# Kernel optimization log

Measured on AMD Instinct MI355X. Metric: run time of the kernel, lower is better.

Reference implementation:

```python
import jax, jax.numpy as jnp
import numpy as np

N = 100000
F = 128
H = 16
C = 40
E = 3200000


def _gcn_norm(edge_index, num_nodes):
    # add self-loops, compute symmetric normalization (PyG GCNConv default)
    loops = jnp.arange(num_nodes, dtype=edge_index.dtype)
    src = jnp.concatenate([edge_index[0], loops])
    dst = jnp.concatenate([edge_index[1], loops])
    ones = jnp.ones(src.shape[0], dtype=jnp.float32)
    deg = jax.ops.segment_sum(ones, dst, num_segments=num_nodes)
    dinv = jnp.where(deg > 0, jax.lax.rsqrt(deg), 0.0)
    norm = dinv[src] * dinv[dst]  # [E+N]
    return src, dst, norm


def _gcn_conv(x, W, b, src, dst, norm, num_nodes):
    h = x @ W                                   # [N, out] transform first (PyG order)
    msg = h[src] * norm[:, None]                # gather + scale
    agg = jax.ops.segment_sum(msg, dst, num_segments=num_nodes)  # scatter-add
    return agg + b


def setup_inputs() -> dict:
    key = jax.random.key(0)
    k = jax.random.split(key, 6)
    x = jax.random.normal(k[0], (N, F), dtype=jnp.float32)
    edge_index = jax.random.randint(k[1], (2, E), 0, N, dtype=jnp.int64)
    W1 = jax.random.normal(k[2], (F, H), dtype=jnp.float32) / np.sqrt(F)
    b1 = jnp.zeros((H,), dtype=jnp.float32)
    W2 = jax.random.normal(k[3], (H, C), dtype=jnp.float32) / np.sqrt(H)
    b2 = jnp.zeros((C,), dtype=jnp.float32)
    return {"x": x, "edge_index": edge_index, "W1": W1, "b1": b1, "W2": W2, "b2": b2}


def reference(x, edge_index, W1, b1, W2, b2):
    src, dst, norm = _gcn_norm(edge_index, N)
    h = _gcn_conv(x, W1, b1, src, dst, norm, N)
    h = jax.nn.relu(h)
    out = _gcn_conv(h, W2, b2, src, dst, norm, N)
    return out
```

## Files before the change

kernel.cpp:

```cpp
#include <hip/hip_runtime.h>
#include <hip/hip_fp16.h>


#define N_NODES 100000
#define F_IN    128
#define H_MID   16
#define C_OUT   40
#define N_EDGES 3200000

#define EC      8192
#define EBLK    391
#define NBUK    391
#define M_HIST  (NBUK * EBLK)
#define NPART   299
#define SRC_MASK 0x1FFFF


__global__ void __launch_bounds__(1024) k_hist(
    const int* __restrict__ dst, int* __restrict__ hist) {
    __shared__ int h[NBUK];
    int t = threadIdx.x, blk = blockIdx.x;
    for (int i = t; i < NBUK; i += 1024) h[i] = 0;
    __syncthreads();
#pragma unroll
    for (int i = 0; i < EC / 1024; ++i) {
        int e = blk * EC + i * 1024 + t;
        if (e < N_EDGES) atomicAdd(&h[dst[e] >> 8], 1);
    }
    __syncthreads();
    for (int b = t; b < NBUK; b += 1024) hist[b * EBLK + blk] = h[b];
}

__global__ void __launch_bounds__(512) k_scanA(int* __restrict__ hist,
                                               int* __restrict__ part) {
    __shared__ int s[512];
    int t = threadIdx.x;
    int i = blockIdx.x * 512 + t;
    int v = (i < M_HIST) ? hist[i] : 0;
    s[t] = v;
    __syncthreads();
    for (int off = 1; off < 512; off <<= 1) {
        int x = (t >= off) ? s[t - off] : 0;
        __syncthreads();
        s[t] += x;
        __syncthreads();
    }
    if (i < M_HIST) hist[i] = s[t] - v;
    if (t == 511) part[blockIdx.x] = s[511];
}

__global__ void __launch_bounds__(512) k_scanB(int* __restrict__ part) {
    __shared__ int s[512];
    int t = threadIdx.x;
    int v = (t < NPART) ? part[t] : 0;
    s[t] = v;
    __syncthreads();
    for (int off = 1; off < 512; off <<= 1) {
        int x = (t >= off) ? s[t - off] : 0;
        __syncthreads();
        s[t] += x;
        __syncthreads();
    }
    if (t < NPART) part[t] = s[t] - v;
}

__global__ void __launch_bounds__(1024) k_part(
    const int* __restrict__ src, const int* __restrict__ dst,
    const int* __restrict__ hist, const int* __restrict__ part,
    int* __restrict__ eb) {
    __shared__ int cur[NBUK];
    int t = threadIdx.x, blk = blockIdx.x;
    for (int b = t; b < NBUK; b += 1024) {
        int idx = b * EBLK + blk;
        cur[b] = hist[idx] + part[idx >> 9];
    }
    __syncthreads();
#pragma unroll
    for (int i = 0; i < EC / 1024; ++i) {
        int e = blk * EC + i * 1024 + t;
        if (e < N_EDGES) {
            int d = dst[e], s = src[e];
            int b = d >> 8;
            int pos = atomicAdd(&cur[b], 1);
            eb[pos] = ((d & 255) << 17) | s;
        }
    }
}

__global__ void __launch_bounds__(512) k_csr(
    const int* __restrict__ hist, const int* __restrict__ part,
    const int* __restrict__ eb,
    int* __restrict__ rp, float* __restrict__ dinv, int* __restrict__ es) {
    __shared__ int deg[256], scn[256], cur[256];
    int b = blockIdx.x, t = threadIdx.x;
    int i0 = b * EBLK;
    int bb = hist[i0] + part[i0 >> 9];
    int bn = (b + 1 < NBUK) ? (hist[i0 + EBLK] + part[(i0 + EBLK) >> 9]) : N_EDGES;
    int ecnt = bn - bb;
    if (t < 256) deg[t] = 0;
    __syncthreads();
    for (int i = t; i < ecnt; i += 512) atomicAdd(&deg[eb[bb + i] >> 17], 1);
    __syncthreads();
    if (t < 256) scn[t] = deg[t];
    __syncthreads();
    for (int off = 1; off < 256; off <<= 1) {
        int x = (t < 256 && t >= off) ? scn[t - off] : 0;
        __syncthreads();
        if (t < 256) scn[t] += x;
        __syncthreads();
    }
    if (t < 256) {
        int ex = scn[t] - deg[t];
        cur[t] = ex;
        int node = b * 256 + t;
        rp[node] = bb + ex;
        dinv[node] = rsqrtf(1.0f + (float)deg[t]);
    }
    __syncthreads();
    for (int i = t; i < ecnt; i += 512) {
        int v = eb[bb + i];
        int r = atomicAdd(&cur[v >> 17], 1);
        es[bb + r] = v & SRC_MASK;
    }
}


__global__ void __launch_bounds__(256) k_gemm1(
    const float* __restrict__ x, const float* __restrict__ W1,
    const float* __restrict__ dinv, __half* __restrict__ h1p) {
    __shared__ float w[F_IN * H_MID];
    __shared__ float xs[16 * 132];
    int t = threadIdx.x;
    for (int i = t; i < F_IN * H_MID; i += 256) w[i] = W1[i];
    int tile = blockIdx.x;
    const float4* xg = (const float4*)(x + (size_t)tile * 16 * F_IN);
    float4* xs4 = (float4*)xs;
    for (int i = t; i < 512; i += 256) {
        int r = i >> 5, c4 = i & 31;
        xs4[r * 33 + c4] = xg[r * 32 + c4];
    }
    __syncthreads();
    int node = t >> 4, j = t & 15;
    const float* xr = xs + node * 132;
    float acc = 0.f;
#pragma unroll 8
    for (int k = 0; k < F_IN; ++k) acc += xr[k] * w[k * H_MID + j];
    int g = tile * 16 + node;
    h1p[(size_t)g * H_MID + j] = __float2half(acc * dinv[g]);
}

__global__ void __launch_bounds__(256) k_gather1(
    const int* __restrict__ rp, const int* __restrict__ es,
    const float* __restrict__ dinv, const __half* __restrict__ h1p,
    const float* __restrict__ b1, __half* __restrict__ r1p) {
    int t = threadIdx.x;
    int node = blockIdx.x * 16 + (t >> 4), j = t & 15;
    float dv = dinv[node];
    int beg = rp[node], end = rp[node + 1];
    float acc = __half2float(h1p[(size_t)node * H_MID + j]);
    int e = beg;
    for (; e + 8 <= end; e += 8) {
        int s0 = es[e],     s1 = es[e + 1], s2 = es[e + 2], s3 = es[e + 3];
        int s4 = es[e + 4], s5 = es[e + 5], s6 = es[e + 6], s7 = es[e + 7];
        __half v0 = h1p[(size_t)s0 * H_MID + j];
        __half v1 = h1p[(size_t)s1 * H_MID + j];
        __half v2 = h1p[(size_t)s2 * H_MID + j];
        __half v3 = h1p[(size_t)s3 * H_MID + j];
        __half v4 = h1p[(size_t)s4 * H_MID + j];
        __half v5 = h1p[(size_t)s5 * H_MID + j];
        __half v6 = h1p[(size_t)s6 * H_MID + j];
        __half v7 = h1p[(size_t)s7 * H_MID + j];
        acc += __half2float(v0) + __half2float(v1) + __half2float(v2) + __half2float(v3)
             + __half2float(v4) + __half2float(v5) + __half2float(v6) + __half2float(v7);
    }
    for (; e < end; ++e) acc += __half2float(h1p[(size_t)es[e] * H_MID + j]);
    float agg1 = dv * acc;
    r1p[(size_t)node * H_MID + j] = __float2half(fmaxf(agg1 + b1[j], 0.f) * dv);
}

__global__ void __launch_bounds__(256) k_gather2(
    const int* __restrict__ rp, const int* __restrict__ es,
    const float* __restrict__ dinv, const __half* __restrict__ r1p,
    const float* __restrict__ W2, const float* __restrict__ b2,
    float* __restrict__ out) {
    __shared__ float w2[H_MID * C_OUT];
    __shared__ float a2[16 * 17];
    int t = threadIdx.x;
    for (int i = t; i < H_MID * C_OUT; i += 256) w2[i] = W2[i];
    int tile = blockIdx.x;
    int node = tile * 16 + (t >> 4), j = t & 15;
    float dv = dinv[node];
    int beg = rp[node], end = rp[node + 1];
    float acc = __half2float(r1p[(size_t)node * H_MID + j]);
    int e = beg;
    for (; e + 8 <= end; e += 8) {
        int s0 = es[e],     s1 = es[e + 1], s2 = es[e + 2], s3 = es[e + 3];
        int s4 = es[e + 4], s5 = es[e + 5], s6 = es[e + 6], s7 = es[e + 7];
        __half v0 = r1p[(size_t)s0 * H_MID + j];
        __half v1 = r1p[(size_t)s1 * H_MID + j];
        __half v2 = r1p[(size_t)s2 * H_MID + j];
        __half v3 = r1p[(size_t)s3 * H_MID + j];
        __half v4 = r1p[(size_t)s4 * H_MID + j];
        __half v5 = r1p[(size_t)s5 * H_MID + j];
        __half v6 = r1p[(size_t)s6 * H_MID + j];
        __half v7 = r1p[(size_t)s7 * H_MID + j];
        acc += __half2float(v0) + __half2float(v1) + __half2float(v2) + __half2float(v3)
             + __half2float(v4) + __half2float(v5) + __half2float(v6) + __half2float(v7);
    }
    for (; e < end; ++e) acc += __half2float(r1p[(size_t)es[e] * H_MID + j]);
    a2[(t >> 4) * 17 + j] = dv * acc;
    __syncthreads();
    for (int idx = t; idx < 16 * C_OUT; idx += 256) {
        int nd = idx / C_OUT, c = idx % C_OUT;
        float s = b2[c];
#pragma unroll
        for (int jj = 0; jj < H_MID; ++jj) s += a2[nd * 17 + jj] * w2[jj * C_OUT + c];
        out[((size_t)tile * 16 + nd) * C_OUT + c] = s;
    }
}

extern "C" void kernel_launch(void* const* d_in, const int* in_sizes, int n_in,
                              void* d_out, int out_size, void* d_ws, size_t ws_size,
                              hipStream_t stream) {
    const float* x  = (const float*)d_in[0];
    const int*   ei = (const int*)d_in[1];
    const float* W1 = (const float*)d_in[2];
    const float* b1 = (const float*)d_in[3];
    const float* W2 = (const float*)d_in[4];
    const float* b2 = (const float*)d_in[5];
    float* out = (float*)d_out;

    const int* src = ei;
    const int* dst = ei + N_EDGES;

    int* rp     = (int*)d_ws;
    float* dinv = (float*)(rp + 100352);
    int* es     = (int*)(dinv + 100352);
    __half* h1p = (__half*)(es + N_EDGES);
    __half* r1p = h1p + (size_t)N_NODES * H_MID;

    int* eb   = (int*)d_out;
    int* hist = eb + N_EDGES;
    int* part = hist + 153088;

    k_hist <<<EBLK, 1024, 0, stream>>>(dst, hist);
    k_scanA<<<NPART, 512, 0, stream>>>(hist, part);
    k_scanB<<<1, 512, 0, stream>>>(part);
    k_part <<<EBLK, 1024, 0, stream>>>(src, dst, hist, part, eb);
    k_csr  <<<NBUK, 512, 0, stream>>>(hist, part, eb, rp, dinv, es);
    k_gemm1<<<N_NODES / 16, 256, 0, stream>>>(x, W1, dinv, h1p);
    k_gather1<<<N_NODES / 16, 256, 0, stream>>>(rp, es, dinv, h1p, b1, r1p);
    k_gather2<<<N_NODES / 16, 256, 0, stream>>>(rp, es, dinv, r1p, W2, b2, out);
}
```

Measured before the change: 241.5 us.

## Stage partition and CSR scatters in LDS, add nontemporal loads/stores

```diff
diff --git a/kernel.cpp b/kernel.cpp
--- a/kernel.cpp
+++ b/kernel.cpp
@@ -14,6 +14,7 @@
 #define M_HIST  (NBUK * EBLK)
 #define NPART   299
 #define SRC_MASK 0x1FFFF
+#define CAP_CSR 10240
 
 
 __global__ void __launch_bounds__(1024) k_hist(
@@ -25,7 +26,7 @@
 #pragma unroll
     for (int i = 0; i < EC / 1024; ++i) {
         int e = blk * EC + i * 1024 + t;
-        if (e < N_EDGES) atomicAdd(&h[dst[e] >> 8], 1);
+        if (e < N_EDGES) atomicAdd(&h[__builtin_nontemporal_load(dst + e) >> 8], 1);
     }
     __syncthreads();
     for (int b = t; b < NBUK; b += 1024) hist[b * EBLK + blk] = h[b];
@@ -68,30 +69,67 @@
     const int* __restrict__ src, const int* __restrict__ dst,
     const int* __restrict__ hist, const int* __restrict__ part,
     int* __restrict__ eb) {
-    __shared__ int cur[NBUK];
+    __shared__ int cnt[NBUK];
+    __shared__ int scn[512];
+    __shared__ int dlt[NBUK];
+    __shared__ int cr[NBUK];
+    __shared__ int sval[EC];
+    __shared__ int spos[EC];
     int t = threadIdx.x, blk = blockIdx.x;
+    for (int b = t; b < NBUK; b += 1024) cnt[b] = 0;
+    __syncthreads();
+    int e0 = blk * EC;
+    int d[8], s[8], bk[8];
+    bool val[8];
+#pragma unroll
+    for (int k = 0; k < 8; ++k) {
+        int e = e0 + k * 1024 + t;
+        val[k] = (e < N_EDGES);
+        d[k] = val[k] ? __builtin_nontemporal_load(dst + e) : 0;
+        s[k] = val[k] ? __builtin_nontemporal_load(src + e) : 0;
+        bk[k] = d[k] >> 8;
+    }
+#pragma unroll
+    for (int k = 0; k < 8; ++k)
+        if (val[k]) atomicAdd(&cnt[bk[k]], 1);
+    __syncthreads();
+    if (t < 512) scn[t] = (t < NBUK) ? cnt[t] : 0;
+    __syncthreads();
+    for (int off = 1; off < 512; off <<= 1) {
+        int x = 0;
+        if (t < 512 && t >= off) x = scn[t - off];
+        __syncthreads();
+        if (t < 512) scn[t] += x;
+        __syncthreads();
+    }
     for (int b = t; b < NBUK; b += 1024) {
         int idx = b * EBLK + blk;
-        cur[b] = hist[idx] + part[idx >> 9];
-    }
-    __syncthreads();
-#pragma unroll
-    for (int i = 0; i < EC / 1024; ++i) {
-        int e = blk * EC + i * 1024 + t;
-        if (e < N_EDGES) {
-            int d = dst[e], s = src[e];
-            int b = d >> 8;
-            int pos = atomicAdd(&cur[b], 1);
-            eb[pos] = ((d & 255) << 17) | s;
+        int gb = hist[idx] + part[idx >> 9];
+        int lb = scn[b] - cnt[b];
+        dlt[b] = gb - lb;
+        cr[b] = lb;
+    }
+    __syncthreads();
+#pragma unroll
+    for (int k = 0; k < 8; ++k) {
+        if (val[k]) {
+            int lr = atomicAdd(&cr[bk[k]], 1);
+            sval[lr] = ((d[k] & 255) << 17) | s[k];
+            spos[lr] = lr + dlt[bk[k]];
         }
     }
+    __syncthreads();
+    int n = (e0 + EC <= N_EDGES) ? EC : (N_EDGES - e0);
+    for (int i = t; i < n; i += 1024)
+        eb[spos[i]] = sval[i];
 }
 
 __global__ void __launch_bounds__(512) k_csr(
     const int* __restrict__ hist, const int* __restrict__ part,
     const int* __restrict__ eb,
     int* __restrict__ rp, float* __restrict__ dinv, int* __restrict__ es) {
-    __shared__ int deg[256], scn[256], cur[256];
+    __shared__ int deg[256], scn[256], cw[256];
+    __shared__ int esl[CAP_CSR];
     int b = blockIdx.x, t = threadIdx.x;
     int i0 = b * EBLK;
     int bb = hist[i0] + part[i0 >> 9];
@@ -99,7 +137,8 @@
     int ecnt = bn - bb;
     if (t < 256) deg[t] = 0;
     __syncthreads();
-    for (int i = t; i < ecnt; i += 512) atomicAdd(&deg[eb[bb + i] >> 17], 1);
+    for (int i = t; i < ecnt; i += 512)
+        atomicAdd(&deg[__builtin_nontemporal_load(eb + bb + i) >> 17], 1);
     __syncthreads();
     if (t < 256) scn[t] = deg[t];
     __syncthreads();
@@ -111,19 +150,32 @@
     }
     if (t < 256) {
         int ex = scn[t] - deg[t];
-        cur[t] = ex;
+        cw[t] = ex;
         int node = b * 256 + t;
         rp[node] = bb + ex;
         dinv[node] = rsqrtf(1.0f + (float)deg[t]);
     }
     __syncthreads();
-    for (int i = t; i < ecnt; i += 512) {
-        int v = eb[bb + i];
-        int r = atomicAdd(&cur[v >> 17], 1);
-        es[bb + r] = v & SRC_MASK;
-    }
-}
-
+    if (ecnt <= CAP_CSR) {
+        for (int i = t; i < ecnt; i += 512) {
+            int v = __builtin_nontemporal_load(eb + bb + i);
+            int r = atomicAdd(&cw[v >> 17], 1);
+            esl[r] = v & SRC_MASK;
+        }
+        __syncthreads();
+        for (int i = t; i < ecnt; i += 512)
+            __builtin_nontemporal_store(esl[i], es + bb + i);
+    } else {
+        for (int i = t; i < ecnt; i += 512) {
+            int v = eb[bb + i];
+            int r = atomicAdd(&cw[v >> 17], 1);
+            es[bb + r] = v & SRC_MASK;
+        }
+    }
+}
+
+
+typedef float f4 __attribute__((ext_vector_type(4)));
 
 __global__ void __launch_bounds__(256) k_gemm1(
     const float* __restrict__ x, const float* __restrict__ W1,
@@ -133,11 +185,11 @@
     int t = threadIdx.x;
     for (int i = t; i < F_IN * H_MID; i += 256) w[i] = W1[i];
     int tile = blockIdx.x;
-    const float4* xg = (const float4*)(x + (size_t)tile * 16 * F_IN);
-    float4* xs4 = (float4*)xs;
+    const f4* xg = (const f4*)(x + (size_t)tile * 16 * F_IN);
+    f4* xs4 = (f4*)xs;
     for (int i = t; i < 512; i += 256) {
         int r = i >> 5, c4 = i & 31;
-        xs4[r * 33 + c4] = xg[r * 32 + c4];
+        xs4[r * 33 + c4] = __builtin_nontemporal_load(xg + r * 32 + c4);
     }
     __syncthreads();
     int node = t >> 4, j = t & 15;
@@ -175,7 +227,8 @@
     }
     for (; e < end; ++e) acc += __half2float(h1p[(size_t)es[e] * H_MID + j]);
     float agg1 = dv * acc;
-    r1p[(size_t)node * H_MID + j] = __float2half(fmaxf(agg1 + b1[j], 0.f) * dv);
+    unsigned short o = __half_as_ushort(__float2half(fmaxf(agg1 + b1[j], 0.f) * dv));
+    __builtin_nontemporal_store(o, (unsigned short*)(r1p + (size_t)node * H_MID + j));
 }
 
 __global__ void __launch_bounds__(256) k_gather2(
@@ -215,7 +268,7 @@
         float s = b2[c];
 #pragma unroll
         for (int jj = 0; jj < H_MID; ++jj) s += a2[nd * 17 + jj] * w2[jj * C_OUT + c];
-        out[((size_t)tile * 16 + nd) * C_OUT + c] = s;
+        __builtin_nontemporal_store(s, &out[((size_t)tile * 16 + nd) * C_OUT + c]);
     }
 }
 
```

Result: faster. 235.3 us (-2.6%).
